# Kernel optimization log

Measured on AMD Instinct MI355X. Metric: run time of the kernel, lower is better.

## Reference

```python
import jax, jax.numpy as jnp
import numpy as np

B, T, C = 2, 2048, 1024
N_HEAD = 16
HEAD_DIM = C // N_HEAD


def setup_inputs() -> dict:
    key = jax.random.key(0)
    k1, k2, k3 = jax.random.split(key, 3)
    s = 1.0 / np.sqrt(C)
    return {
        "x": jax.random.normal(k1, (B, T, C), dtype=jnp.float32),
        "w_qkv": jax.random.normal(k2, (C, 3 * C), dtype=jnp.float32) * s,
        "b_qkv": jnp.zeros((3 * C,), dtype=jnp.float32),
        "w_out": jax.random.normal(k3, (C, C), dtype=jnp.float32) * s,
        "b_out": jnp.zeros((C,), dtype=jnp.float32),
    }


def reference(x, w_qkv, b_qkv, w_out, b_out):
    b, t, c = x.shape
    qkv = x @ w_qkv + b_qkv                                   # [B,T,3C]
    # Faithful to torch: view(B,T,H,3*hd).transpose(1,2) then split last dim
    qkv = qkv.reshape(b, t, N_HEAD, 3 * HEAD_DIM).transpose(0, 2, 1, 3)  # [B,H,T,3hd]
    q, k, v = jnp.split(qkv, 3, axis=-1)                      # each [B,H,T,hd]
    att = jnp.einsum("bhqd,bhkd->bhqk", q, k) / np.sqrt(HEAD_DIM)
    causal = jnp.tril(jnp.ones((t, t), dtype=bool))
    att = jnp.where(causal[None, None], att, -jnp.inf)
    att = jax.nn.softmax(att, axis=-1)                        # dropout p=0 (eval)
    y = jnp.einsum("bhqk,bhkd->bhqd", att, v)                 # [B,H,T,hd]
    y = y.transpose(0, 2, 1, 3).reshape(b, t, c)
    return y @ w_out + b_out
```

## Files before the change

### kernel.cpp

```cpp
#include <hip/hip_runtime.h>


#define T_SEQ 2048
#define C_DIM 1024
#define NH    16
#define HD    64
#define BT    4096

typedef short bf16x8 __attribute__((ext_vector_type(8)));
typedef float floatx4 __attribute__((ext_vector_type(4)));

static __device__ __forceinline__ unsigned short f2bf(float f) {
    union { float f; unsigned u; } v; v.f = f;
    unsigned u = v.u;
    return (unsigned short)((u + 0x7FFFu + ((u >> 16) & 1u)) >> 16);
}

static __device__ __forceinline__ void gl2lds16(const void* g, void* l) {
    __builtin_amdgcn_global_load_lds(
        (const __attribute__((address_space(1))) unsigned int*)g,
        (__attribute__((address_space(3))) unsigned int*)l, 16, 0, 0);
}

static __device__ __forceinline__ void transpose_body(float (*tile)[65],
                                                      const float* __restrict__ W,
                                                      unsigned short* __restrict__ Wt,
                                                      int K, int N, int bx, int by) {
    const int k0 = by << 6;
    const int n0 = bx << 6;
    const int rr = threadIdx.x >> 4;
    const int cc = (threadIdx.x & 15) << 2;
#pragma unroll
    for (int i = 0; i < 4; i++) {
        int r = rr + (i << 4);
        *(float4*)&tile[r][cc] = *(const float4*)(W + (size_t)(k0 + r) * N + n0 + cc);
    }
    __syncthreads();
#pragma unroll
    for (int i = 0; i < 4; i++) {
        int nr = rr + (i << 4);
        ushort4 o;
        o.x = f2bf(tile[cc + 0][nr]);
        o.y = f2bf(tile[cc + 1][nr]);
        o.z = f2bf(tile[cc + 2][nr]);
        o.w = f2bf(tile[cc + 3][nr]);
        *(ushort4*)(Wt + (size_t)(n0 + nr) * K + k0 + cc) = o;
    }
}

__global__ __launch_bounds__(256) void prep(const float* __restrict__ x,
                                            unsigned short* __restrict__ xb,
                                            const float* __restrict__ w_qkv,
                                            unsigned short* __restrict__ wqkvT,
                                            const float* __restrict__ w_out,
                                            unsigned short* __restrict__ woutT) {
    __shared__ float tile[64][65];
    const int bx = blockIdx.x;
    if (bx < 1024) {
        int i = (bx * 256 + threadIdx.x) * 4;
        const int n = BT * C_DIM;
        const int stride = 1024 * 1024;
        for (; i < n; i += stride) {
            float4 f = *(const float4*)(x + i);
            ushort4 o;
            o.x = f2bf(f.x); o.y = f2bf(f.y); o.z = f2bf(f.z); o.w = f2bf(f.w);
            *(ushort4*)(xb + i) = o;
        }
    } else if (bx < 1024 + 768) {
        int b = bx - 1024;
        transpose_body(tile, w_qkv, wqkvT, 1024, 3072, b % 48, b / 48);
    } else {
        int b = bx - 1024 - 768;
        transpose_body(tile, w_out, woutT, 1024, 1024, b % 16, b / 16);
    }
}

__global__ __launch_bounds__(256) void transp_v(const unsigned short* __restrict__ vb,
                                                unsigned short* __restrict__ vt) {
    __shared__ unsigned short tile[64][68];
    const int t0 = blockIdx.x << 6;
    const int bh = blockIdx.y;
    const size_t base = (size_t)bh * T_SEQ * HD;
    const int r = threadIdx.x >> 3;
    const int c = (threadIdx.x & 7) << 3;
#pragma unroll
    for (int i = 0; i < 2; i++) {
        const unsigned short* src = vb + base + (size_t)(t0 + r + (i << 5)) * HD + c;
        ushort4 u0 = *(const ushort4*)src;
        ushort4 u1 = *(const ushort4*)(src + 4);
        *(ushort4*)&tile[r + (i << 5)][c] = u0;
        *(ushort4*)&tile[r + (i << 5)][c + 4] = u1;
    }
    __syncthreads();
#pragma unroll
    for (int i = 0; i < 2; i++) {
        int s = threadIdx.x + (i << 8);
        int d = s >> 3;
        int tc = (s & 7) << 3;
        ushort4 o0, o1;
        o0.x = tile[tc + 0][d]; o0.y = tile[tc + 1][d];
        o0.z = tile[tc + 2][d]; o0.w = tile[tc + 3][d];
        o1.x = tile[tc + 4][d]; o1.y = tile[tc + 5][d];
        o1.z = tile[tc + 6][d]; o1.w = tile[tc + 7][d];
        unsigned short* dst = vt + ((size_t)bh * HD + d) * T_SEQ + t0 + tc;
        *(ushort4*)dst = o0;
        *(ushort4*)(dst + 4) = o1;
    }
}

#define GEMM_CORE(A_, Bt_, K_)                                                      \
    __shared__ short As[128 * 64];                                                  \
    __shared__ short Bs[128 * 64];                                                  \
    const int tid  = threadIdx.x;                                                   \
    const int lane = tid & 63, wave = tid >> 6;                                     \
    const int ln   = lane & 15, quad = lane >> 4;                                   \
    const int wm   = wave & 1,  wn   = wave >> 1;                                   \
    const int row0 = blockIdx.y << 7;                                               \
    const int col0 = blockIdx.x << 7;                                               \
    floatx4 acc[4][4];                                                              \
    _Pragma("unroll")                                                               \
    for (int i = 0; i < 4; i++)                                                     \
        _Pragma("unroll")                                                           \
        for (int j = 0; j < 4; j++) acc[i][j] = (floatx4){0.f, 0.f, 0.f, 0.f};      \
    for (int k0 = 0; k0 < K_; k0 += 64) {                                           \
        _Pragma("unroll")                                                           \
        for (int i = 0; i < 4; i++) {                                               \
            int c = (i << 8) + tid;                                                 \
            int r = c >> 3;                                                         \
            int gsrc = (c & 7) ^ (r & 7);                                           \
            gl2lds16(A_  + (size_t)(row0 + r) * K_ + k0 + (gsrc << 3), &As[c << 3]); \
            gl2lds16(Bt_ + (size_t)(col0 + r) * K_ + k0 + (gsrc << 3), &Bs[c << 3]); \
        }                                                                           \
        __syncthreads();                                                            \
        _Pragma("unroll")                                                           \
        for (int half = 0; half < 2; half++) {                                      \
            bf16x8 af[4], bfr[4];                                                   \
            _Pragma("unroll")                                                       \
            for (int t4 = 0; t4 < 4; t4++) {                                        \
                int ra = (wm << 6) + (t4 << 4) + ln;                                \
                int rb = (wn << 6) + (t4 << 4) + ln;                                \
                int g  = (half << 2) + quad;                                        \
                af[t4]  = *(bf16x8*)&As[((ra << 3) + (g ^ (ra & 7))) << 3];         \
                bfr[t4] = *(bf16x8*)&Bs[((rb << 3) + (g ^ (rb & 7))) << 3];         \
            }                                                                       \
            _Pragma("unroll")                                                       \
            for (int mt = 0; mt < 4; mt++)                                          \
                _Pragma("unroll")                                                   \
                for (int nt = 0; nt < 4; nt++)                                      \
                    acc[mt][nt] = __builtin_amdgcn_mfma_f32_16x16x32_bf16(af[mt], bfr[nt], acc[mt][nt], 0, 0, 0); \
        }                                                                           \
        __syncthreads();                                                            \
    }

__global__ __launch_bounds__(256) void gemm_qkv(const unsigned short* __restrict__ A,
                                                const unsigned short* __restrict__ Bt,
                                                const float* __restrict__ bias,
                                                unsigned short* __restrict__ qb,
                                                unsigned short* __restrict__ kb,
                                                unsigned short* __restrict__ vb) {
    GEMM_CORE(A, Bt, 1024)
#pragma unroll
    for (int mt = 0; mt < 4; mt++) {
#pragma unroll
        for (int nt = 0; nt < 4; nt++) {
            int n = col0 + (wn << 6) + (nt << 4) + ln;
            int h = n / 192, r = n % 192;
            int sel = r >> 6, d = r & 63;
            float bv = bias[n];
#pragma unroll
            for (int e = 0; e < 4; e++) {
                int m = row0 + (wm << 6) + (mt << 4) + (quad << 2) + e;
                int b = m >> 11, t = m & 2047;
                float val = acc[mt][nt][e] + bv;
                size_t idx = (((size_t)(b * NH + h)) * T_SEQ + t) * HD + d;
                if (sel == 0)
                    qb[idx] = f2bf(val * 0.125f);
                else if (sel == 1)
                    kb[idx] = f2bf(val);
                else
                    vb[idx] = f2bf(val);
            }
        }
    }
}

__global__ __launch_bounds__(256) void gemm_out(const unsigned short* __restrict__ A,
                                                const unsigned short* __restrict__ Bt,
                                                const float* __restrict__ bias,
                                                float* __restrict__ out) {
    GEMM_CORE(A, Bt, 1024)
    const int N = 1024;
#pragma unroll
    for (int mt = 0; mt < 4; mt++) {
#pragma unroll
        for (int nt = 0; nt < 4; nt++) {
            int n = col0 + (wn << 6) + (nt << 4) + ln;
            float bv = bias[n];
#pragma unroll
            for (int e = 0; e < 4; e++) {
                int m = row0 + (wm << 6) + (mt << 4) + (quad << 2) + e;
                out[(size_t)m * N + n] = acc[mt][nt][e] + bv;
            }
        }
    }
}

__global__ __launch_bounds__(256, 4) void attn(const unsigned short* __restrict__ qb,
                                               const unsigned short* __restrict__ kb,
                                               const unsigned short* __restrict__ vt,
                                               unsigned short* __restrict__ y) {
    __shared__ short Ks[64][72];
    __shared__ short Vs[64][72];
    __shared__ short QP[64][72];
    const int tid  = threadIdx.x;
    const int w    = tid >> 6, lane = tid & 63;
    const int ln   = lane & 15, quad = lane >> 4;
    const int qt   = 31 - (int)blockIdx.x;
    const int bh   = blockIdx.y;
    const size_t base = (size_t)bh * T_SEQ * HD;
    const int q0   = qt << 6;
    const int sb   = q0 + (w << 4);
    const float NEG_INF = -__builtin_inff();

    const int sr = tid >> 3;
    const int sc = (tid & 7) << 3;

    bf16x8 qtmp[2], kreg[2], vreg[2];
#pragma unroll
    for (int i = 0; i < 2; i++) {
        qtmp[i] = *(const bf16x8*)(qb + base + (size_t)(q0 + sr + (i << 5)) * HD + sc);
        kreg[i] = *(const bf16x8*)(kb + base + (size_t)(sr + (i << 5)) * HD + sc);
        vreg[i] = *(const bf16x8*)(vt + base + (size_t)(sr + (i << 5)) * T_SEQ + sc);
    }
#pragma unroll
    for (int i = 0; i < 2; i++) *(bf16x8*)&QP[sr + (i << 5)][sc] = qtmp[i];
    __syncthreads();

    bf16x8 bq0 = *(bf16x8*)&QP[(w << 4) + ln][quad << 3];
    bf16x8 bq1 = *(bf16x8*)&QP[(w << 4) + ln][32 + (quad << 3)];

    floatx4 o[4];
#pragma unroll
    for (int nt = 0; nt < 4; nt++) o[nt] = (floatx4){0.f, 0.f, 0.f, 0.f};
    float m_prev = NEG_INF, l_run = 0.f;

    for (int kt = 0; kt <= qt; kt++) {
        const int k0 = kt << 6;
        __syncthreads();
#pragma unroll
        for (int i = 0; i < 2; i++) {
            *(bf16x8*)&Ks[sr + (i << 5)][sc] = kreg[i];
            *(bf16x8*)&Vs[sr + (i << 5)][sc] = vreg[i];
        }
        __syncthreads();
        if (kt < qt) {
            const int kn = k0 + 64;
#pragma unroll
            for (int i = 0; i < 2; i++) {
                kreg[i] = *(const bf16x8*)(kb + base + (size_t)(kn + sr + (i << 5)) * HD + sc);
                vreg[i] = *(const bf16x8*)(vt + base + (size_t)(sr + (i << 5)) * T_SEQ + kn + sc);
            }
        }

        const bool diag  = (kt == qt);
        const int  nlive = diag ? w : 3;

        floatx4 st[4];
#pragma unroll
        for (int ktl = 0; ktl < 4; ktl++) {
            if (ktl <= nlive) {
                bf16x8 a0 = *(bf16x8*)&Ks[(ktl << 4) + ln][quad << 3];
                bf16x8 a1 = *(bf16x8*)&Ks[(ktl << 4) + ln][32 + (quad << 3)];
                floatx4 acc = (floatx4){0.f, 0.f, 0.f, 0.f};
                acc = __builtin_amdgcn_mfma_f32_16x16x32_bf16(a0, bq0, acc, 0, 0, 0);
                acc = __builtin_amdgcn_mfma_f32_16x16x32_bf16(a1, bq1, acc, 0, 0, 0);
                st[ktl] = acc;
            }
        }
        if (diag) {
#pragma unroll
            for (int ktl = 0; ktl < 4; ktl++) {
                if (ktl <= nlive) {
#pragma unroll
                    for (int e = 0; e < 4; e++) {
                        int kg = k0 + (ktl << 4) + (quad << 2) + e;
                        if (kg > sb + ln) st[ktl][e] = NEG_INF;
                    }
                }
            }
        }

        float mx = NEG_INF;
#pragma unroll
        for (int ktl = 0; ktl < 4; ktl++)
            if (ktl <= nlive) {
#pragma unroll
                for (int e = 0; e < 4; e++) mx = fmaxf(mx, st[ktl][e]);
            }
        mx = fmaxf(mx, __shfl_xor(mx, 16));
        mx = fmaxf(mx, __shfl_xor(mx, 32));
        float m_new = fmaxf(m_prev, mx);
        float alpha = __expf(m_prev - m_new);
        float psum = 0.f;
#pragma unroll
        for (int ktl = 0; ktl < 4; ktl++)
            if (ktl <= nlive) {
#pragma unroll
                for (int e = 0; e < 4; e++) {
                    float p = __expf(st[ktl][e] - m_new);
                    st[ktl][e] = p;
                    psum += p;
                }
            }
        psum += __shfl_xor(psum, 16);
        psum += __shfl_xor(psum, 32);
        l_run = l_run * alpha + psum;
        m_prev = m_new;

#pragma unroll
        for (int ktl = 0; ktl < 4; ktl++) {
            ushort4 pw;
            if (ktl <= nlive) {
                pw.x = f2bf(st[ktl][0]); pw.y = f2bf(st[ktl][1]);
                pw.z = f2bf(st[ktl][2]); pw.w = f2bf(st[ktl][3]);
            } else {
                pw.x = 0; pw.y = 0; pw.z = 0; pw.w = 0;
            }
            *(ushort4*)&QP[(w << 4) + ln][(ktl << 4) + (quad << 2)] = pw;
        }

        float arow[4];
#pragma unroll
        for (int e = 0; e < 4; e++) arow[e] = __shfl(alpha, (quad << 2) + e);
#pragma unroll
        for (int nt = 0; nt < 4; nt++)
#pragma unroll
            for (int e = 0; e < 4; e++) o[nt][e] *= arow[e];

        bf16x8 ap0 = *(bf16x8*)&QP[(w << 4) + ln][quad << 3];
        bf16x8 ap1 = *(bf16x8*)&QP[(w << 4) + ln][32 + (quad << 3)];
#pragma unroll
        for (int nt = 0; nt < 4; nt++) {
            bf16x8 v0 = *(bf16x8*)&Vs[(nt << 4) + ln][quad << 3];
            bf16x8 v1 = *(bf16x8*)&Vs[(nt << 4) + ln][32 + (quad << 3)];
            o[nt] = __builtin_amdgcn_mfma_f32_16x16x32_bf16(ap0, v0, o[nt], 0, 0, 0);
            o[nt] = __builtin_amdgcn_mfma_f32_16x16x32_bf16(ap1, v1, o[nt], 0, 0, 0);
        }
    }

    float linv[4];
#pragma unroll
    for (int e = 0; e < 4; e++) linv[e] = 1.0f / __shfl(l_run, (quad << 2) + e);
    const int b = bh >> 4, h = bh & 15;
#pragma unroll
    for (int e = 0; e < 4; e++) {
        int t = sb + (quad << 2) + e;
        unsigned short* yrow = y + ((size_t)b * T_SEQ + t) * C_DIM + h * HD;
#pragma unroll
        for (int nt = 0; nt < 4; nt++)
            yrow[(nt << 4) + ln] = f2bf(o[nt][e] * linv[e]);
    }
}

extern "C" void kernel_launch(void* const* d_in, const int* in_sizes, int n_in,
                              void* d_out, int out_size, void* d_ws, size_t ws_size,
                              hipStream_t stream) {
    (void)in_sizes; (void)n_in; (void)out_size; (void)ws_size;
    const float* x     = (const float*)d_in[0];
    const float* w_qkv = (const float*)d_in[1];
    const float* b_qkv = (const float*)d_in[2];
    const float* w_out = (const float*)d_in[3];
    const float* b_out = (const float*)d_in[4];
    float* out = (float*)d_out;

    char* ws = (char*)d_ws;
    unsigned short* qb    = (unsigned short*)ws;
    unsigned short* kb    = (unsigned short*)(ws + ((size_t)8  << 20));
    unsigned short* vb    = (unsigned short*)(ws + ((size_t)16 << 20));
    unsigned short* vt    = (unsigned short*)(ws + ((size_t)24 << 20));
    unsigned short* xb    = (unsigned short*)(ws + ((size_t)32 << 20));
    unsigned short* yb    = xb;
    unsigned short* wqkvT = (unsigned short*)(ws + ((size_t)40 << 20));
    unsigned short* woutT = (unsigned short*)(ws + ((size_t)46 << 20));

    prep    <<<2048, 256, 0, stream>>>(x, xb, w_qkv, wqkvT, w_out, woutT);
    gemm_qkv<<<dim3(24, 32), 256, 0, stream>>>(xb, wqkvT, b_qkv, qb, kb, vb);
    transp_v<<<dim3(32, 32), 256, 0, stream>>>(vb, vt);
    attn    <<<dim3(32, 32), 256, 0, stream>>>(qb, kb, vt, yb);
    gemm_out<<<dim3(8, 32), 256, 0, stream>>>(yb, woutT, b_out, out);
}
```

Before: 232.1 us.

## Load K and V MFMA fragments directly from global memory, dropping shared tiles

```diff
diff --git a/kernel.cpp b/kernel.cpp
--- a/kernel.cpp
+++ b/kernel.cpp
@@ -209,9 +209,7 @@
                                                const unsigned short* __restrict__ kb,
                                                const unsigned short* __restrict__ vt,
                                                unsigned short* __restrict__ y) {
-    __shared__ short Ks[64][72];
-    __shared__ short Vs[64][72];
-    __shared__ short QP[64][72];
+    __shared__ short P[64][72];
     const int tid  = threadIdx.x;
     const int w    = tid >> 6, lane = tid & 63;
     const int ln   = lane & 15, quad = lane >> 4;
@@ -222,22 +220,9 @@
     const int sb   = q0 + (w << 4);
     const float NEG_INF = -__builtin_inff();
 
-    const int sr = tid >> 3;
-    const int sc = (tid & 7) << 3;
-
-    bf16x8 qtmp[2], kreg[2], vreg[2];
-#pragma unroll
-    for (int i = 0; i < 2; i++) {
-        qtmp[i] = *(const bf16x8*)(qb + base + (size_t)(q0 + sr + (i << 5)) * HD + sc);
-        kreg[i] = *(const bf16x8*)(kb + base + (size_t)(sr + (i << 5)) * HD + sc);
-        vreg[i] = *(const bf16x8*)(vt + base + (size_t)(sr + (i << 5)) * T_SEQ + sc);
-    }
-#pragma unroll
-    for (int i = 0; i < 2; i++) *(bf16x8*)&QP[sr + (i << 5)][sc] = qtmp[i];
-    __syncthreads();
-
-    bf16x8 bq0 = *(bf16x8*)&QP[(w << 4) + ln][quad << 3];
-    bf16x8 bq1 = *(bf16x8*)&QP[(w << 4) + ln][32 + (quad << 3)];
+    const unsigned short* qrow = qb + base + (size_t)(sb + ln) * HD;
+    const bf16x8 bq0 = *(const bf16x8*)(qrow + (quad << 3));
+    const bf16x8 bq1 = *(const bf16x8*)(qrow + 32 + (quad << 3));
 
     floatx4 o[4];
 #pragma unroll
@@ -246,31 +231,24 @@
 
     for (int kt = 0; kt <= qt; kt++) {
         const int k0 = kt << 6;
-        __syncthreads();
-#pragma unroll
-        for (int i = 0; i < 2; i++) {
-            *(bf16x8*)&Ks[sr + (i << 5)][sc] = kreg[i];
-            *(bf16x8*)&Vs[sr + (i << 5)][sc] = vreg[i];
-        }
-        __syncthreads();
-        if (kt < qt) {
-            const int kn = k0 + 64;
-#pragma unroll
-            for (int i = 0; i < 2; i++) {
-                kreg[i] = *(const bf16x8*)(kb + base + (size_t)(kn + sr + (i << 5)) * HD + sc);
-                vreg[i] = *(const bf16x8*)(vt + base + (size_t)(sr + (i << 5)) * T_SEQ + kn + sc);
-            }
-        }
-
         const bool diag  = (kt == qt);
         const int  nlive = diag ? w : 3;
 
+        bf16x8 vf0[4], vf1[4];
+#pragma unroll
+        for (int nt = 0; nt < 4; nt++) {
+            const unsigned short* vrow = vt + base + (size_t)((nt << 4) + ln) * T_SEQ + k0;
+            vf0[nt] = *(const bf16x8*)(vrow + (quad << 3));
+            vf1[nt] = *(const bf16x8*)(vrow + 32 + (quad << 3));
+        }
+
         floatx4 st[4];
 #pragma unroll
         for (int ktl = 0; ktl < 4; ktl++) {
             if (ktl <= nlive) {
-                bf16x8 a0 = *(bf16x8*)&Ks[(ktl << 4) + ln][quad << 3];
-                bf16x8 a1 = *(bf16x8*)&Ks[(ktl << 4) + ln][32 + (quad << 3)];
+                const unsigned short* krow = kb + base + (size_t)(k0 + (ktl << 4) + ln) * HD;
+                bf16x8 a0 = *(const bf16x8*)(krow + (quad << 3));
+                bf16x8 a1 = *(const bf16x8*)(krow + 32 + (quad << 3));
                 floatx4 acc = (floatx4){0.f, 0.f, 0.f, 0.f};
                 acc = __builtin_amdgcn_mfma_f32_16x16x32_bf16(a0, bq0, acc, 0, 0, 0);
                 acc = __builtin_amdgcn_mfma_f32_16x16x32_bf16(a1, bq1, acc, 0, 0, 0);
@@ -326,7 +304,7 @@
             } else {
                 pw.x = 0; pw.y = 0; pw.z = 0; pw.w = 0;
             }
-            *(ushort4*)&QP[(w << 4) + ln][(ktl << 4) + (quad << 2)] = pw;
+            *(ushort4*)&P[(w << 4) + ln][(ktl << 4) + (quad << 2)] = pw;
         }
 
         float arow[4];
@@ -337,14 +315,12 @@
 #pragma unroll
             for (int e = 0; e < 4; e++) o[nt][e] *= arow[e];
 
-        bf16x8 ap0 = *(bf16x8*)&QP[(w << 4) + ln][quad << 3];
-        bf16x8 ap1 = *(bf16x8*)&QP[(w << 4) + ln][32 + (quad << 3)];
+        bf16x8 ap0 = *(bf16x8*)&P[(w << 4) + ln][quad << 3];
+        bf16x8 ap1 = *(bf16x8*)&P[(w << 4) + ln][32 + (quad << 3)];
 #pragma unroll
         for (int nt = 0; nt < 4; nt++) {
-            bf16x8 v0 = *(bf16x8*)&Vs[(nt << 4) + ln][quad << 3];
-            bf16x8 v1 = *(bf16x8*)&Vs[(nt << 4) + ln][32 + (quad << 3)];
-            o[nt] = __builtin_amdgcn_mfma_f32_16x16x32_bf16(ap0, v0, o[nt], 0, 0, 0);
-            o[nt] = __builtin_amdgcn_mfma_f32_16x16x32_bf16(ap1, v1, o[nt], 0, 0, 0);
+            o[nt] = __builtin_amdgcn_mfma_f32_16x16x32_bf16(ap0, vf0[nt], o[nt], 0, 0, 0);
+            o[nt] = __builtin_amdgcn_mfma_f32_16x16x32_bf16(ap1, vf1[nt], o[nt], 0, 0, 0);
         }
     }
 
```

After: 378.5 us. +63.1%, slower.

## Split long causal attention rows into two KV chunks and retile output GEMM

Applied to the files above, without the earlier changes.

```diff
diff --git a/kernel.cpp b/kernel.cpp
--- a/kernel.cpp
+++ b/kernel.cpp
@@ -14,6 +14,9 @@
     union { float f; unsigned u; } v; v.f = f;
     unsigned u = v.u;
     return (unsigned short)((u + 0x7FFFu + ((u >> 16) & 1u)) >> 16);
+}
+static __device__ __forceinline__ float bf2f(unsigned short u) {
+    union { unsigned u; float f; } v; v.u = ((unsigned)u) << 16; return v.f;
 }
 
 static __device__ __forceinline__ void gl2lds16(const void* g, void* l) {
@@ -188,13 +191,64 @@
                                                 const unsigned short* __restrict__ Bt,
                                                 const float* __restrict__ bias,
                                                 float* __restrict__ out) {
-    GEMM_CORE(A, Bt, 1024)
-    const int N = 1024;
+    const int K = 1024, N = 1024;
+    __shared__ short As[128 * 64];
+    __shared__ short Bs[64 * 64];
+    const int tid  = threadIdx.x;
+    const int lane = tid & 63, wave = tid >> 6;
+    const int ln   = lane & 15, quad = lane >> 4;
+    const int wm   = wave & 1,  wn   = wave >> 1;
+    const int row0 = blockIdx.y << 7;
+    const int col0 = blockIdx.x << 6;
+    floatx4 acc[4][2];
+#pragma unroll
+    for (int i = 0; i < 4; i++)
+#pragma unroll
+        for (int j = 0; j < 2; j++) acc[i][j] = (floatx4){0.f, 0.f, 0.f, 0.f};
+    for (int k0 = 0; k0 < K; k0 += 64) {
+#pragma unroll
+        for (int i = 0; i < 4; i++) {
+            int c = (i << 8) + tid;
+            int r = c >> 3;
+            int gsrc = (c & 7) ^ (r & 7);
+            gl2lds16(A + (size_t)(row0 + r) * K + k0 + (gsrc << 3), &As[c << 3]);
+        }
+#pragma unroll
+        for (int i = 0; i < 2; i++) {
+            int c = (i << 8) + tid;
+            int r = c >> 3;
+            int gsrc = (c & 7) ^ (r & 7);
+            gl2lds16(Bt + (size_t)(col0 + r) * K + k0 + (gsrc << 3), &Bs[c << 3]);
+        }
+        __syncthreads();
+#pragma unroll
+        for (int half = 0; half < 2; half++) {
+            bf16x8 af[4], bfr[2];
+#pragma unroll
+            for (int t4 = 0; t4 < 4; t4++) {
+                int ra = (wm << 6) + (t4 << 4) + ln;
+                int g  = (half << 2) + quad;
+                af[t4] = *(bf16x8*)&As[((ra << 3) + (g ^ (ra & 7))) << 3];
+            }
+#pragma unroll
+            for (int t2 = 0; t2 < 2; t2++) {
+                int rb = (wn << 5) + (t2 << 4) + ln;
+                int g  = (half << 2) + quad;
+                bfr[t2] = *(bf16x8*)&Bs[((rb << 3) + (g ^ (rb & 7))) << 3];
+            }
+#pragma unroll
+            for (int mt = 0; mt < 4; mt++)
+#pragma unroll
+                for (int nt = 0; nt < 2; nt++)
+                    acc[mt][nt] = __builtin_amdgcn_mfma_f32_16x16x32_bf16(af[mt], bfr[nt], acc[mt][nt], 0, 0, 0);
+        }
+        __syncthreads();
+    }
 #pragma unroll
     for (int mt = 0; mt < 4; mt++) {
 #pragma unroll
-        for (int nt = 0; nt < 4; nt++) {
-            int n = col0 + (wn << 6) + (nt << 4) + ln;
+        for (int nt = 0; nt < 2; nt++) {
+            int n = col0 + (wn << 5) + (nt << 4) + ln;
             float bv = bias[n];
 #pragma unroll
             for (int e = 0; e < 4; e++) {
@@ -205,17 +259,25 @@
     }
 }
 
-__global__ __launch_bounds__(256, 4) void attn(const unsigned short* __restrict__ qb,
-                                               const unsigned short* __restrict__ kb,
-                                               const unsigned short* __restrict__ vt,
-                                               unsigned short* __restrict__ y) {
+__global__ __launch_bounds__(256, 4) void attn_p1(const unsigned short* __restrict__ qb,
+                                                  const unsigned short* __restrict__ kb,
+                                                  const unsigned short* __restrict__ vt,
+                                                  unsigned short* __restrict__ y,
+                                                  unsigned short* __restrict__ po,
+                                                  float* __restrict__ pm,
+                                                  float* __restrict__ pl) {
     __shared__ short Ks[64][72];
     __shared__ short Vs[64][72];
     __shared__ short QP[64][72];
     const int tid  = threadIdx.x;
     const int w    = tid >> 6, lane = tid & 63;
     const int ln   = lane & 15, quad = lane >> 4;
-    const int qt   = 31 - (int)blockIdx.x;
+    const int bx   = blockIdx.x;
+    int qt, cidx, kt_lo; bool fin;
+    if (bx < 16)      { qt = 31 - bx;        cidx = 0; kt_lo = 0;  fin = false; }
+    else if (bx < 32) { qt = 31 - (bx - 16); cidx = 1; kt_lo = 16; fin = false; }
+    else              { qt = 15 - (bx - 32); cidx = 0; kt_lo = 0;  fin = true;  }
+    const int kt_hi = (!fin && cidx == 0) ? 15 : qt;
     const int bh   = blockIdx.y;
     const size_t base = (size_t)bh * T_SEQ * HD;
     const int q0   = qt << 6;
@@ -226,11 +288,12 @@
     const int sc = (tid & 7) << 3;
 
     bf16x8 qtmp[2], kreg[2], vreg[2];
+    const int kk0 = kt_lo << 6;
 #pragma unroll
     for (int i = 0; i < 2; i++) {
         qtmp[i] = *(const bf16x8*)(qb + base + (size_t)(q0 + sr + (i << 5)) * HD + sc);
-        kreg[i] = *(const bf16x8*)(kb + base + (size_t)(sr + (i << 5)) * HD + sc);
-        vreg[i] = *(const bf16x8*)(vt + base + (size_t)(sr + (i << 5)) * T_SEQ + sc);
+        kreg[i] = *(const bf16x8*)(kb + base + (size_t)(kk0 + sr + (i << 5)) * HD + sc);
+        vreg[i] = *(const bf16x8*)(vt + base + (size_t)(sr + (i << 5)) * T_SEQ + kk0 + sc);
     }
 #pragma unroll
     for (int i = 0; i < 2; i++) *(bf16x8*)&QP[sr + (i << 5)][sc] = qtmp[i];
@@ -244,7 +307,7 @@
     for (int nt = 0; nt < 4; nt++) o[nt] = (floatx4){0.f, 0.f, 0.f, 0.f};
     float m_prev = NEG_INF, l_run = 0.f;
 
-    for (int kt = 0; kt <= qt; kt++) {
+    for (int kt = kt_lo; kt <= kt_hi; kt++) {
         const int k0 = kt << 6;
         __syncthreads();
 #pragma unroll
@@ -253,7 +316,7 @@
             *(bf16x8*)&Vs[sr + (i << 5)][sc] = vreg[i];
         }
         __syncthreads();
-        if (kt < qt) {
+        if (kt < kt_hi) {
             const int kn = k0 + 64;
 #pragma unroll
             for (int i = 0; i < 2; i++) {
@@ -348,17 +411,67 @@
         }
     }
 
-    float linv[4];
-#pragma unroll
-    for (int e = 0; e < 4; e++) linv[e] = 1.0f / __shfl(l_run, (quad << 2) + e);
+    if (fin) {
+        float linv[4];
+#pragma unroll
+        for (int e = 0; e < 4; e++) linv[e] = 1.0f / __shfl(l_run, (quad << 2) + e);
+        const int b = bh >> 4, h = bh & 15;
+#pragma unroll
+        for (int e = 0; e < 4; e++) {
+            int t = sb + (quad << 2) + e;
+            unsigned short* yrow = y + ((size_t)b * T_SEQ + t) * C_DIM + h * HD;
+#pragma unroll
+            for (int nt = 0; nt < 4; nt++)
+                yrow[(nt << 4) + ln] = f2bf(o[nt][e] * linv[e]);
+        }
+    } else {
+        const int slot = (((bh << 4) + (qt - 16)) << 1) + cidx;
+        if (quad == 0) {
+            pm[(slot << 6) + (w << 4) + ln] = m_prev;
+            pl[(slot << 6) + (w << 4) + ln] = l_run;
+        }
+#pragma unroll
+        for (int e = 0; e < 4; e++) {
+            int q = (w << 4) + (quad << 2) + e;
+            unsigned short* porow = po + (((size_t)slot << 6) + q) * HD;
+#pragma unroll
+            for (int nt = 0; nt < 4; nt++)
+                porow[(nt << 4) + ln] = f2bf(o[nt][e]);
+        }
+    }
+}
+
+__global__ __launch_bounds__(256) void attn_p2(const unsigned short* __restrict__ po,
+                                               const float* __restrict__ pm,
+                                               const float* __restrict__ pl,
+                                               unsigned short* __restrict__ y) {
+    const int qt = 16 + blockIdx.x;
+    const int bh = blockIdx.y;
+    const int slot0 = ((bh << 4) + (qt - 16)) << 1;
+    const int tid = threadIdx.x;
+    const int q  = tid >> 2;
+    const int d0 = (tid & 3) << 4;
+    float m0 = pm[(slot0 << 6) + q], m1 = pm[((slot0 + 1) << 6) + q];
+    float l0 = pl[(slot0 << 6) + q], l1 = pl[((slot0 + 1) << 6) + q];
+    float m  = fmaxf(m0, m1);
+    float a0 = __expf(m0 - m), a1 = __expf(m1 - m);
+    float inv = 1.0f / (l0 * a0 + l1 * a1);
+    a0 *= inv; a1 *= inv;
+    const unsigned short* r0 = po + (((size_t)slot0 << 6) + q) * HD + d0;
+    const unsigned short* r1 = po + (((size_t)(slot0 + 1) << 6) + q) * HD + d0;
     const int b = bh >> 4, h = bh & 15;
-#pragma unroll
-    for (int e = 0; e < 4; e++) {
-        int t = sb + (quad << 2) + e;
-        unsigned short* yrow = y + ((size_t)b * T_SEQ + t) * C_DIM + h * HD;
-#pragma unroll
-        for (int nt = 0; nt < 4; nt++)
-            yrow[(nt << 4) + ln] = f2bf(o[nt][e] * linv[e]);
+    const int t = (qt << 6) + q;
+    unsigned short* yrow = y + ((size_t)b * T_SEQ + t) * C_DIM + h * HD + d0;
+#pragma unroll
+    for (int i = 0; i < 4; i++) {
+        ushort4 u0 = *(const ushort4*)(r0 + (i << 2));
+        ushort4 u1 = *(const ushort4*)(r1 + (i << 2));
+        ushort4 ow;
+        ow.x = f2bf(bf2f(u0.x) * a0 + bf2f(u1.x) * a1);
+        ow.y = f2bf(bf2f(u0.y) * a0 + bf2f(u1.y) * a1);
+        ow.z = f2bf(bf2f(u0.z) * a0 + bf2f(u1.z) * a1);
+        ow.w = f2bf(bf2f(u0.w) * a0 + bf2f(u1.w) * a1);
+        *(ushort4*)(yrow + (i << 2)) = ow;
     }
 }
 
@@ -382,10 +495,14 @@
     unsigned short* yb    = xb;
     unsigned short* wqkvT = (unsigned short*)(ws + ((size_t)40 << 20));
     unsigned short* woutT = (unsigned short*)(ws + ((size_t)46 << 20));
+    unsigned short* po    = (unsigned short*)(ws + ((size_t)48 << 20));
+    float*          pm    = (float*)(ws + ((size_t)56 << 20));
+    float*          pl    = (float*)(ws + ((size_t)56 << 20) + (256 << 10));
 
     prep    <<<2048, 256, 0, stream>>>(x, xb, w_qkv, wqkvT, w_out, woutT);
     gemm_qkv<<<dim3(24, 32), 256, 0, stream>>>(xb, wqkvT, b_qkv, qb, kb, vb);
     transp_v<<<dim3(32, 32), 256, 0, stream>>>(vb, vt);
-    attn    <<<dim3(32, 32), 256, 0, stream>>>(qb, kb, vt, yb);
-    gemm_out<<<dim3(8, 32), 256, 0, stream>>>(yb, woutT, b_out, out);
-}
+    attn_p1 <<<dim3(48, 32), 256, 0, stream>>>(qb, kb, vt, yb, po, pm, pl);
+    attn_p2 <<<dim3(16, 32), 256, 0, stream>>>(po, pm, pl, yb);
+    gemm_out<<<dim3(16, 32), 256, 0, stream>>>(yb, woutT, b_out, out);
+}
```

New measurement: 210.1 us. -9.5%, faster.
